# Kernel optimization log

Measured on AMD Instinct MI355X. Metric: run time of the kernel, lower is better.

## Reference

```python
import jax, jax.numpy as jnp
import numpy as np

NC = 13   # num_classes
NA = 5    # num_anchors
COORD_SCALE = 1.0
NOOBJECT_SCALE = 0.1
CLASS_SCALE = 1.0


def setup_inputs() -> dict:
    key = jax.random.key(0)
    k1, k2, k3 = jax.random.split(key, 3)
    nB, nH, nW = 32, 76, 76
    output = jax.random.normal(k1, (nB, NA * (19 + NC), nH, nW), dtype=jnp.float32)
    # target: channel 0 = class id (0 == background), channels 1..18 = nine (gx,gy)
    # keypoint coordinates in grid units.
    cls_t = jax.random.randint(k2, (nB, NA, nH, nW, 1), 0, NC).astype(jnp.float32)
    coords_t = jax.random.uniform(k3, (nB, NA, nH, nW, 18), dtype=jnp.float32) * nW
    target = jnp.concatenate([cls_t, coords_t], axis=-1)
    return {"output": output, "target": target}


def _region_loss(output, target):
    nB, nH, nW = output.shape[0], output.shape[2], output.shape[3]
    out = output.reshape(nB, NA, 19 + NC, nH, nW)
    cls_logits = out[:, :, :NC]          # [B,A,C,H,W]
    conf = out[:, :, NC]                 # [B,A,H,W] (raw, no sigmoid in source)
    coords = out[:, :, NC + 1:]          # [B,A,18,H,W]
    xs = coords[:, :, 0::2]              # [B,A,9,H,W]
    ys = coords[:, :, 1::2]
    # only the first keypoint (x0,y0) is passed through sigmoid in the source
    xs = jnp.concatenate([jax.nn.sigmoid(xs[:, :, :1]), xs[:, :, 1:]], axis=2)
    ys = jnp.concatenate([jax.nn.sigmoid(ys[:, :, :1]), ys[:, :, 1:]], axis=2)

    grid_x = jnp.arange(nW, dtype=output.dtype)             # broadcasts on W
    grid_y = jnp.arange(nH, dtype=output.dtype)[:, None]    # broadcasts on H

    # ground-truth keypoints -> cell-relative offsets (tx = gx - w, ty = gy - h)
    g = target[..., 1:].reshape(nB, NA, nH, nW, 9, 2)
    gx = jnp.transpose(g[..., 0], (0, 1, 4, 2, 3))          # [B,A,9,H,W]
    gy = jnp.transpose(g[..., 1], (0, 1, 4, 2, 3))
    txs = gx - grid_x
    tys = gy - grid_y

    # pred_boxes were built from .data in torch -> detached
    pxs = jax.lax.stop_gradient(xs + grid_x)
    pys = jax.lax.stop_gradient(ys + grid_y)

    # compute_conf: exp(2 - d/15) if d < 30 else 0, averaged over the 9 points
    dt = jnp.sqrt((txs - pxs) ** 2 + (tys - pys) ** 2)
    tconf = jnp.where(dt < 30.0, jnp.exp(2.0 - dt / 15.0), 0.0).mean(axis=2)

    obj = target[..., 0] != 0                                # [B,A,H,W]
    coor_mask = obj.astype(output.dtype)[:, :, None]         # [B,A,1,H,W]

    # coordinate loss: sum over 9 keypoints of MSE(x*m, tx*m)/2 (sum reduction)
    loss_coord = 0.5 * COORD_SCALE * (
        jnp.sum((coor_mask * (xs - txs)) ** 2)
        + jnp.sum((coor_mask * (ys - tys)) ** 2)
    )

    # confidence loss; conf_mask is uniformly noobject_scale in the source
    loss_conf = 0.5 * jnp.sum((NOOBJECT_SCALE * (conf - tconf)) ** 2)

    # class loss: sum-reduced cross entropy over object cells
    logp = jax.nn.log_softmax(cls_logits, axis=2)            # [B,A,C,H,W]
    tcls = target[..., 0].astype(jnp.int32)                  # [B,A,H,W]
    nll = -jnp.take_along_axis(logp, tcls[:, :, None], axis=2)[:, :, 0]
    loss_cls = CLASS_SCALE * jnp.sum(jnp.where(obj, nll, 0.0))

    return loss_coord + loss_conf + loss_cls


def reference(output, target):
    return _region_loss(output, target)
```

## Files before the change

### kernel.cpp

```cpp
#include <hip/hip_runtime.h>


namespace {

constexpr int kNC = 13;
constexpr int kCh = 32;
constexpr int kH = 76, kW = 76;
constexpr int kSP = kH * kW;
constexpr int kCells = 32 * 5 * kSP;
constexpr int kCPB = 512;
constexpr int kBlocks = kCells / kCPB;
constexpr int kSlabW = kCPB * 19;
constexpr int kSlabF4 = kSlabW / 4;

__device__ __forceinline__ float comp2(const float2& v, int j) {
  return j == 0 ? v.x : v.y;
}

__global__ __launch_bounds__(256, 4)
void region_loss_v4(const float* __restrict__ out,
                    const float* __restrict__ tgt,
                    double* __restrict__ acc)
{
  __shared__ float tl[kSlabW];
  const int tid = threadIdx.x;
  const int blk = blockIdx.x;

  const float* tg = tgt + (size_t)blk * kSlabW;
  float4 st[9];
#pragma unroll
  for (int i = 0; i < 9; ++i)
    st[i] = *(const float4*)(tg + (size_t)(tid + i * 256) * 4);
  float4 stTail;
  const bool hasTail = tid < (kSlabF4 - 9 * 256);
  if (hasTail) stTail = *(const float4*)(tg + (size_t)(tid + 9 * 256) * 4);
#pragma unroll
  for (int i = 0; i < 9; ++i)
    *(float4*)(&tl[(tid + i * 256) * 4]) = st[i];
  if (hasTail) *(float4*)(&tl[(tid + 9 * 256) * 4]) = stTail;

  const int n0 = blk * kCPB + tid * 2;
  const int q  = n0 / kSP;
  const int s0 = n0 - q * kSP;
  const float* op = out + (size_t)q * kCh * kSP + s0;

  float fw[2], fh[2];
#pragma unroll
  for (int j = 0; j < 2; ++j) {
    const int s = s0 + j;
    const int hh = s / kW;
    fh[j] = (float)hh;
    fw[j] = (float)(s - hh * kW);
  }

  float2 L[kNC];
#pragma unroll
  for (int c = 0; c < kNC; ++c)
    L[c] = *(const float2*)(op + (size_t)c * kSP);
  const float2 CF = *(const float2*)(op + (size_t)kNC * kSP);
  float2 X[9], Y[9];
#pragma unroll
  for (int i = 0; i < 9; ++i) {
    X[i] = *(const float2*)(op + (size_t)(14 + 2 * i) * kSP);
    Y[i] = *(const float2*)(op + (size_t)(15 + 2 * i) * kSP);
  }

  __syncthreads();

  const int r0 = tid * 2 * 19;
  float loss[2] = {0.f, 0.f};

#pragma unroll
  for (int j = 0; j < 2; ++j) {
    const int rb = r0 + j * 19;
    const float clsf = tl[rb];
    const bool obj = (clsf != 0.f);

    float tcf = 0.f, lcd = 0.f;
#pragma unroll
    for (int i = 0; i < 9; ++i) {
      float xv = comp2(X[i], j), yv = comp2(Y[i], j);
      if (i == 0) {
        xv = __builtin_amdgcn_rcpf(1.f + __expf(-xv));
        yv = __builtin_amdgcn_rcpf(1.f + __expf(-yv));
      }
      const float gx = tl[rb + 1 + 2 * i];
      const float gy = tl[rb + 2 + 2 * i];
      const float tx = gx - fw[j];
      const float ty = gy - fh[j];
      const float dx = tx - (xv + fw[j]);
      const float dy = ty - (yv + fh[j]);
      const float dt = sqrtf(dx * dx + dy * dy);
      if (dt < 30.f) tcf += __expf(2.f - dt * (1.f / 15.f));
      const float ex = xv - tx;
      const float ey = yv - ty;
      lcd += ex * ex + ey * ey;
    }

    const float d = comp2(CF, j) - tcf * (1.f / 9.f);
    loss[j] = 0.005f * d * d;
    if (obj) loss[j] += 0.5f * lcd;

    if (obj) {
      float mx = comp2(L[0], j);
#pragma unroll
      for (int c = 1; c < kNC; ++c) mx = fmaxf(mx, comp2(L[c], j));
      float se = 0.f;
#pragma unroll
      for (int c = 0; c < kNC; ++c) se += __expf(comp2(L[c], j) - mx);
      const int tc = (int)clsf;
      float sel = 0.f;
#pragma unroll
      for (int c = 0; c < kNC; ++c) sel += (c == tc) ? comp2(L[c], j) : 0.f;
      loss[j] += -(sel - mx - __logf(se));
    }
  }

  float lsum = loss[0] + loss[1];
#pragma unroll
  for (int off = 32; off > 0; off >>= 1)
    lsum += __shfl_down(lsum, off, 64);

  __shared__ float wsum[4];
  const int lane = tid & 63;
  const int wid = tid >> 6;
  if (lane == 0) wsum[wid] = lsum;
  __syncthreads();
  if (tid == 0)
    atomicAdd(acc, (double)(wsum[0] + wsum[1] + wsum[2] + wsum[3]));
}

__global__ void finalize_kernel(const double* __restrict__ acc,
                                float* __restrict__ outv)
{
  outv[0] = (float)acc[0];
}

}

extern "C" void kernel_launch(void* const* d_in, const int* in_sizes, int n_in,
                              void* d_out, int out_size, void* d_ws, size_t ws_size,
                              hipStream_t stream) {
  const float* output = (const float*)d_in[0];
  const float* target = (const float*)d_in[1];
  double* acc = (double*)d_ws;

  hipMemsetAsync(acc, 0, sizeof(double), stream);

  region_loss_v4<<<kBlocks, 256, 0, stream>>>(output, target, acc);
  finalize_kernel<<<1, 1, 0, stream>>>(acc, (float*)d_out);
}
```

Before: 47.69 us.

## Stage output channels and targets into LDS via direct global-to-LDS loads

Rewrites the memory-transfer plan so each block handles 256 cells, one per thread, instead of 512. All 32 output channels and the target slab are copied straight into shared memory with global_load_lds (4- and 16-byte variants), skipping the register round-trip. Compute then reads operands from LDS. This is meant to cut register pressure and lift memory-level parallelism, at the cost of more LDS per block (about 51KB), a lower occupancy hint, twice as many blocks and atomics, and reliance on the exact lane-to-address layout of the LDS-direct loads.

```diff
diff --git a/kernel.cpp b/kernel.cpp
--- a/kernel.cpp
+++ b/kernel.cpp
@@ -8,123 +8,108 @@
 constexpr int kH = 76, kW = 76;
 constexpr int kSP = kH * kW;
 constexpr int kCells = 32 * 5 * kSP;
-constexpr int kCPB = 512;
-constexpr int kBlocks = kCells / kCPB;
-constexpr int kSlabW = kCPB * 19;
-constexpr int kSlabF4 = kSlabW / 4;
+constexpr int kBlocks = kCells / 256;
+constexpr int kTW = 256 * 19;
 
-__device__ __forceinline__ float comp2(const float2& v, int j) {
-  return j == 0 ? v.x : v.y;
+__device__ __forceinline__ void gl4(const float* g, float* l) {
+  __builtin_amdgcn_global_load_lds(
+      (const __attribute__((address_space(1))) void*)g,
+      (__attribute__((address_space(3))) void*)l, 4, 0, 0);
+}
+__device__ __forceinline__ void gl16(const float* g, float* l) {
+  __builtin_amdgcn_global_load_lds(
+      (const __attribute__((address_space(1))) void*)g,
+      (__attribute__((address_space(3))) void*)l, 16, 0, 0);
 }
 
-__global__ __launch_bounds__(256, 4)
-void region_loss_v4(const float* __restrict__ out,
+__global__ __launch_bounds__(256, 3)
+void region_loss_v5(const float* __restrict__ out,
                     const float* __restrict__ tgt,
                     double* __restrict__ acc)
 {
-  __shared__ float tl[kSlabW];
-  const int tid = threadIdx.x;
-  const int blk = blockIdx.x;
+  __shared__ __align__(16) float ch[kCh][256];
+  __shared__ __align__(16) float tl[kTW];
+  __shared__ float wsum[4];
 
-  const float* tg = tgt + (size_t)blk * kSlabW;
-  float4 st[9];
+  const int tid  = threadIdx.x;
+  const int blk  = blockIdx.x;
+  const int lane = tid & 63;
+  const int w    = tid >> 6;
+  const int wbase = w * 64;
+
+  const int n = blk * 256 + tid;
+  const int q = n / kSP;
+  const int s = n - q * kSP;
+  const float* op = out + (size_t)q * kCh * kSP + s;
+
 #pragma unroll
-  for (int i = 0; i < 9; ++i)
-    st[i] = *(const float4*)(tg + (size_t)(tid + i * 256) * 4);
-  float4 stTail;
-  const bool hasTail = tid < (kSlabF4 - 9 * 256);
-  if (hasTail) stTail = *(const float4*)(tg + (size_t)(tid + 9 * 256) * 4);
+  for (int c = 0; c < kCh; ++c)
+    gl4(op + (size_t)c * kSP, &ch[c][wbase]);
+
+  const float* tg = tgt + (size_t)blk * kTW;
 #pragma unroll
-  for (int i = 0; i < 9; ++i)
-    *(float4*)(&tl[(tid + i * 256) * 4]) = st[i];
-  if (hasTail) *(float4*)(&tl[(tid + 9 * 256) * 4]) = stTail;
-
-  const int n0 = blk * kCPB + tid * 2;
-  const int q  = n0 / kSP;
-  const int s0 = n0 - q * kSP;
-  const float* op = out + (size_t)q * kCh * kSP + s0;
-
-  float fw[2], fh[2];
+  for (int k = 0; k < 4; ++k)
+    gl16(tg + w * 1216 + k * 256 + lane * 4, &tl[w * 1216 + k * 256]);
 #pragma unroll
-  for (int j = 0; j < 2; ++j) {
-    const int s = s0 + j;
-    const int hh = s / kW;
-    fh[j] = (float)hh;
-    fw[j] = (float)(s - hh * kW);
-  }
-
-  float2 L[kNC];
-#pragma unroll
-  for (int c = 0; c < kNC; ++c)
-    L[c] = *(const float2*)(op + (size_t)c * kSP);
-  const float2 CF = *(const float2*)(op + (size_t)kNC * kSP);
-  float2 X[9], Y[9];
-#pragma unroll
-  for (int i = 0; i < 9; ++i) {
-    X[i] = *(const float2*)(op + (size_t)(14 + 2 * i) * kSP);
-    Y[i] = *(const float2*)(op + (size_t)(15 + 2 * i) * kSP);
-  }
+  for (int r = 0; r < 3; ++r)
+    gl4(tg + w * 1216 + 1024 + r * 64 + lane, &tl[w * 1216 + 1024 + r * 64]);
 
   __syncthreads();
 
-  const int r0 = tid * 2 * 19;
-  float loss[2] = {0.f, 0.f};
+  const int hh = s / kW;
+  const float fh = (float)hh;
+  const float fw = (float)(s - hh * kW);
+
+  const int rb = tid * 19;
+  const float clsf = tl[rb];
+  const bool obj = (clsf != 0.f);
+
+  float tcf = 0.f, lcd = 0.f;
+#pragma unroll
+  for (int i = 0; i < 9; ++i) {
+    float xv = ch[14 + 2 * i][tid];
+    float yv = ch[15 + 2 * i][tid];
+    if (i == 0) {
+      xv = __builtin_amdgcn_rcpf(1.f + __expf(-xv));
+      yv = __builtin_amdgcn_rcpf(1.f + __expf(-yv));
+    }
+    const float gx = tl[rb + 1 + 2 * i];
+    const float gy = tl[rb + 2 + 2 * i];
+    const float tx = gx - fw;
+    const float ty = gy - fh;
+    const float dx = tx - (xv + fw);
+    const float dy = ty - (yv + fh);
+    const float dt = sqrtf(dx * dx + dy * dy);
+    if (dt < 30.f) tcf += __expf(2.f - dt * (1.f / 15.f));
+    const float ex = xv - tx;
+    const float ey = yv - ty;
+    lcd += ex * ex + ey * ey;
+  }
+
+  const float conf = ch[kNC][tid];
+  const float d = conf - tcf * (1.f / 9.f);
+  float loss = 0.005f * d * d;
+  if (obj) loss += 0.5f * lcd;
+
+  if (obj) {
+    float mx = ch[0][tid];
+#pragma unroll
+    for (int c = 1; c < kNC; ++c) mx = fmaxf(mx, ch[c][tid]);
+    float se = 0.f;
+#pragma unroll
+    for (int c = 0; c < kNC; ++c) se += __expf(ch[c][tid] - mx);
+    const int tc = (int)clsf;
+    float sel = 0.f;
+#pragma unroll
+    for (int c = 0; c < kNC; ++c) sel += (c == tc) ? ch[c][tid] : 0.f;
+    loss += -(sel - mx - __logf(se));
+  }
 
 #pragma unroll
-  for (int j = 0; j < 2; ++j) {
-    const int rb = r0 + j * 19;
-    const float clsf = tl[rb];
-    const bool obj = (clsf != 0.f);
+  for (int off = 32; off > 0; off >>= 1)
+    loss += __shfl_down(loss, off, 64);
 
-    float tcf = 0.f, lcd = 0.f;
-#pragma unroll
-    for (int i = 0; i < 9; ++i) {
-      float xv = comp2(X[i], j), yv = comp2(Y[i], j);
-      if (i == 0) {
-        xv = __builtin_amdgcn_rcpf(1.f + __expf(-xv));
-        yv = __builtin_amdgcn_rcpf(1.f + __expf(-yv));
-      }
-      const float gx = tl[rb + 1 + 2 * i];
-      const float gy = tl[rb + 2 + 2 * i];
-      const float tx = gx - fw[j];
-      const float ty = gy - fh[j];
-      const float dx = tx - (xv + fw[j]);
-      const float dy = ty - (yv + fh[j]);
-      const float dt = sqrtf(dx * dx + dy * dy);
-      if (dt < 30.f) tcf += __expf(2.f - dt * (1.f / 15.f));
-      const float ex = xv - tx;
-      const float ey = yv - ty;
-      lcd += ex * ex + ey * ey;
-    }
-
-    const float d = comp2(CF, j) - tcf * (1.f / 9.f);
-    loss[j] = 0.005f * d * d;
-    if (obj) loss[j] += 0.5f * lcd;
-
-    if (obj) {
-      float mx = comp2(L[0], j);
-#pragma unroll
-      for (int c = 1; c < kNC; ++c) mx = fmaxf(mx, comp2(L[c], j));
-      float se = 0.f;
-#pragma unroll
-      for (int c = 0; c < kNC; ++c) se += __expf(comp2(L[c], j) - mx);
-      const int tc = (int)clsf;
-      float sel = 0.f;
-#pragma unroll
-      for (int c = 0; c < kNC; ++c) sel += (c == tc) ? comp2(L[c], j) : 0.f;
-      loss[j] += -(sel - mx - __logf(se));
-    }
-  }
-
-  float lsum = loss[0] + loss[1];
-#pragma unroll
-  for (int off = 32; off > 0; off >>= 1)
-    lsum += __shfl_down(lsum, off, 64);
-
-  __shared__ float wsum[4];
-  const int lane = tid & 63;
-  const int wid = tid >> 6;
-  if (lane == 0) wsum[wid] = lsum;
+  if (lane == 0) wsum[w] = loss;
   __syncthreads();
   if (tid == 0)
     atomicAdd(acc, (double)(wsum[0] + wsum[1] + wsum[2] + wsum[3]));
@@ -147,6 +132,6 @@
 
   hipMemsetAsync(acc, 0, sizeof(double), stream);
 
-  region_loss_v4<<<kBlocks, 256, 0, stream>>>(output, target, acc);
+  region_loss_v5<<<kBlocks, 256, 0, stream>>>(output, target, acc);
   finalize_kernel<<<1, 1, 0, stream>>>(acc, (float*)d_out);
 }
```

Result: slower. 64.24 us (+34.7%).
